# Kernel optimization log

Measured on AMD Instinct MI355X. Metric: run time of the kernel, lower is better.

## Reference

```python
import jax, jax.numpy as jnp
import numpy as np
from jax import lax

NPOINT = 1024
NSAMPLE = 32
RADIUS = 0.2
ALPHA = 0.2  # leaky relu slope


def fps(xyz, npoint):
    """Farthest point sampling. xyz: (B,N,3) -> idx (B,npoint) int32."""
    B, N, _ = xyz.shape
    first = jnp.zeros((B,), dtype=jnp.int32)
    dist0 = jnp.full((B, N), 1e10, dtype=xyz.dtype)

    def step(carry, _):
        dist, last = carry
        lp = jnp.take_along_axis(xyz, last[:, None, None], axis=1)  # (B,1,3)
        nd = jnp.sum((xyz - lp) ** 2, axis=-1)                      # (B,N)
        dist = jnp.minimum(dist, nd)
        nxt = jnp.argmax(dist, axis=-1).astype(jnp.int32)
        return (dist, nxt), nxt

    (_, _), idxs = lax.scan(step, (dist0, first), None, length=npoint - 1)
    return jnp.concatenate([first[:, None], idxs.T], axis=1)  # (B,npoint)


def ball_query(xyz, new_xyz, radius, nsample):
    """First-nsample-in-index-order neighbors within radius. -> idx (B,n,k) int32."""
    B, N, _ = xyz.shape
    d2 = (jnp.sum(new_xyz ** 2, -1)[:, :, None]
          + jnp.sum(xyz ** 2, -1)[:, None, :]
          - 2.0 * jnp.einsum('bnc,bmc->bnm', new_xyz, xyz))  # (B,n,N)
    mask = d2 <= radius * radius
    cand = jnp.where(mask, jnp.arange(N, dtype=jnp.int32)[None, None, :], N)
    srt = jnp.sort(cand, axis=-1)[..., :nsample]             # (B,n,k)
    first = srt[..., :1]
    idx = jnp.where(srt == N, first, srt)                     # pad with first valid
    return jnp.minimum(idx, N - 1).astype(jnp.int32)


def feature_enhance(g, f, gn, fn):
    """g(B,n,3) f(B,n,D) gn(B,n,k,3) fn(B,n,k,D) -> (B,n,k,3*3+1+(D+3)*3+1)."""
    # cal_feature_dis: scale neighbor xyz by exp(-mean |f - fn|)
    d = jnp.abs(f[:, :, None, :] - fn)                        # (B,n,k,D)
    fdist = jnp.exp(-jnp.mean(d, axis=-1, keepdims=True))     # (B,n,k,1)
    gn = gn * fdist                                           # broadcast == torch.repeat
    # avg_g: append softmax-geometry residual to features
    gmean = jnp.mean(gn, axis=2)                              # (B,n,3)
    gd = jnp.abs(jax.nn.softmax(gmean, -1) - jax.nn.softmax(g, -1))  # (B,n,3)
    gd = jnp.broadcast_to(gd[:, :, None, :], fn.shape[:3] + (3,))    # (B,n,k,3)
    fn = jnp.concatenate([fn, gd], axis=-1)                   # (B,n,k,D+3)
    f = jnp.concatenate([f, g], axis=-1)                      # (B,n,D+3)
    pg = jnp.broadcast_to(g[:, :, None, :], gn.shape)
    pf = jnp.broadcast_to(f[:, :, None, :], fn.shape)
    pg1 = pg - gn
    pf1 = pf - fn
    dg = jnp.sqrt(jnp.sum(pg1 ** 2, axis=-1, keepdims=True))
    df = jnp.sqrt(jnp.sum(pf1 ** 2, axis=-1, keepdims=True))
    pg2 = jnp.concatenate([gn, pg, pg1, dg], axis=-1)         # (B,n,k,10)
    pf2 = jnp.concatenate([fn, pf, pf1, df], axis=-1)         # (B,n,k,3(D+3)+1)
    return jnp.concatenate([pg2, pf2], axis=-1)


def hetero_attention(nfn, a, w1, b1):
    """Attention pooling over neighbors. nfn (B,n,k,nc) -> (B,n,c).
    (In the original, dgf->Conv2d 'disf' is computed but never used; omitted.)
    Dropout skipped (eval mode)."""
    e = jax.nn.leaky_relu(jnp.einsum('bnkc,cd->bnkd', nfn, a), ALPHA)
    attn = jax.nn.softmax(e, axis=2)                          # over k (dim=2)
    pooled = jnp.sum(attn * nfn, axis=2)                      # (B,n,nc)
    return jnp.einsum('bnc,oc->bno', pooled, w1) + b1         # 1x1 Conv1d


def setup_inputs() -> dict:
    key = jax.random.key(0)
    k1, k2, k3, k4 = jax.random.split(key, 4)
    B, N, D = 8, 4096, 64
    nc, c_out = 212, 128  # nc = 3*3+1 + 3*(D+3)+1
    xyz = jax.random.uniform(k1, (B, N, 3), dtype=jnp.float32)
    features = jax.random.normal(k2, (B, D, N), dtype=jnp.float32)
    xav = 1.414 * np.sqrt(6.0 / (nc + nc))
    a = jax.random.uniform(k3, (nc, nc), minval=-xav, maxval=xav, dtype=jnp.float32)
    w1 = jax.random.normal(k4, (c_out, nc), dtype=jnp.float32) / np.sqrt(nc)
    b1 = jnp.zeros((c_out,), dtype=jnp.float32)
    return {"xyz": xyz, "features": features, "a": a, "w1": w1, "b1": b1}


def reference(xyz, features, a, w1, b1):
    B, N, _ = xyz.shape
    feat = jnp.transpose(features, (0, 2, 1))                 # (B,N,D)
    fps_idx = fps(xyz, NPOINT)                                # (B,n)
    bidx = jnp.arange(B)[:, None]
    new_xyz = xyz[bidx, fps_idx]                              # (B,n,3)
    f = feat[bidx, fps_idx]                                   # (B,n,D)
    nb_idx = ball_query(xyz, new_xyz, RADIUS, NSAMPLE)        # (B,n,k)
    bidx2 = jnp.arange(B)[:, None, None]
    gn = xyz[bidx2, nb_idx]                                   # (B,n,k,3)
    fn = feat[bidx2, nb_idx]                                  # (B,n,k,D)
    nfn = feature_enhance(new_xyz, f, gn, fn)                 # (B,n,k,212)
    new_features = hetero_attention(nfn, a, w1, b1)           # (B,n,c)
    return new_xyz, jnp.transpose(new_features, (0, 2, 1))    # (B,c,n)
```

## Files before the change

### kernel.cpp

```cpp
#include <hip/hip_runtime.h>
#include <hip/hip_bf16.h>

#define B_    8
#define N_    4096
#define D_    64
#define NP_   1024
#define K_    32
#define NC_   212
#define CO_   128
#define FPS_T 256
#define SVW   72
#define PROWS 139

__device__ __forceinline__ float f32add(float a, float b) { return __fadd_rn(a, b); }
__device__ __forceinline__ float f32sub(float a, float b) { return __fsub_rn(a, b); }
__device__ __forceinline__ float f32mul(float a, float b) { return __fmul_rn(a, b); }

__device__ __forceinline__ void waveArgmaxDpp(float& best, int& bidx) {
#define AMAX_STEP(CTRL)                                                                     \
    {                                                                                       \
        int _v = __builtin_amdgcn_update_dpp(__float_as_int(best), __float_as_int(best),    \
                                             (CTRL), 0xf, 0xf, false);                      \
        int _i = __builtin_amdgcn_update_dpp(bidx, bidx, (CTRL), 0xf, 0xf, false);          \
        float _f = __int_as_float(_v);                                                      \
        if (_f > best || (_f == best && _i < bidx)) { best = _f; bidx = _i; }               \
    }
    AMAX_STEP(0x111);
    AMAX_STEP(0x112);
    AMAX_STEP(0x114);
    AMAX_STEP(0x118);
    AMAX_STEP(0x142);
    AMAX_STEP(0x143);
#undef AMAX_STEP
    best = __int_as_float(__builtin_amdgcn_readlane(__float_as_int(best), 63));
    bidx = __builtin_amdgcn_readlane(bidx, 63);
}

__global__ void fold_kernel(const float* __restrict__ A, float* __restrict__ P) {
    int x = blockIdx.x * 256 + threadIdx.x;
    if (x >= PROWS * NC_) return;
    int r = x / NC_, c = x % NC_;
    float v;
    if      (r < 64)  v = A[(size_t)(77 + r) * NC_ + c] + A[(size_t)(144 + r) * NC_ + c];
    else if (r < 67)  { int j = r - 64;
                        v = (A[(size_t)(3 + j) * NC_ + c] + A[(size_t)(141 + j) * NC_ + c])
                          + A[(size_t)(208 + j) * NC_ + c]; }
    else if (r < 70)  { int j = r - 67;
                        v = A[(size_t)(74 + j) * NC_ + c] - A[(size_t)(208 + j) * NC_ + c]; }
    else if (r < 73)  { int j = r - 70;
                        v = A[(size_t)j * NC_ + c] - A[(size_t)(6 + j) * NC_ + c]; }
    else if (r == 73) v = A[(size_t)9 * NC_ + c];
    else if (r < 138) { int i = r - 74;
                        v = A[(size_t)(10 + i) * NC_ + c] - A[(size_t)(144 + i) * NC_ + c]; }
    else              v = A[(size_t)211 * NC_ + c];
    P[(size_t)r * NC_ + c] = v;
}

__global__ void transpose_kernel(const float* __restrict__ in, float* __restrict__ out) {
    __shared__ float tile[32][33];
    int b  = blockIdx.z;
    int n0 = blockIdx.x * 32, d0 = blockIdx.y * 32;
    const float* src = in  + (size_t)b * D_ * N_;
    float*       dst = out + (size_t)b * N_ * D_;
    int tx = threadIdx.x, ty = threadIdx.y;
#pragma unroll
    for (int r = 0; r < 32; r += 8)
        tile[r + ty][tx] = src[(size_t)(d0 + r + ty) * N_ + n0 + tx];
    __syncthreads();
#pragma unroll
    for (int r = 0; r < 32; r += 8)
        dst[(size_t)(n0 + r + ty) * D_ + d0 + tx] = tile[tx][r + ty];
}

__global__ __launch_bounds__(FPS_T) void fps_kernel(
    const float* __restrict__ xyz,
    int* __restrict__ fpsIdx, float* __restrict__ out0) {
    int b = blockIdx.x;
    const float* P = xyz + (size_t)b * N_ * 3;
    __shared__ float X[N_], Y[N_], Z[N_];
    __shared__ int   hist[NP_];
    __shared__ float redV[2][FPS_T / 64];
    __shared__ int   redI[2][FPS_T / 64];
    int tid = threadIdx.x;
    for (int i = tid; i < N_; i += FPS_T) {
        X[i] = P[i * 3 + 0];
        Y[i] = P[i * 3 + 1];
        Z[i] = P[i * 3 + 2];
    }
    if (tid == 0) hist[0] = 0;
    __syncthreads();

    const int PPT = N_ / FPS_T;
    float px[PPT], py[PPT], pz[PPT], dist[PPT];
#pragma unroll
    for (int c = 0; c < PPT; c++) {
        int j = tid + FPS_T * c;
        px[c] = X[j]; py[c] = Y[j]; pz[c] = Z[j];
        dist[c] = 1e10f;
    }
    int last = 0;
    for (int it = 1; it < NP_; ++it) {
        float lx = X[last], ly = Y[last], lz = Z[last];
        float best = -1.0f; int bidx = 0;
#pragma unroll
        for (int c = 0; c < PPT; c++) {
            float dx = f32sub(px[c], lx), dy = f32sub(py[c], ly), dz = f32sub(pz[c], lz);
            float nd = f32add(f32add(f32mul(dx, dx), f32mul(dy, dy)), f32mul(dz, dz));
            float d  = fminf(dist[c], nd);
            dist[c] = d;
            if (d > best) { best = d; bidx = tid + FPS_T * c; }
        }
        waveArgmaxDpp(best, bidx);
        int par = it & 1;
        if ((tid & 63) == 0) { redV[par][tid >> 6] = best; redI[par][tid >> 6] = bidx; }
        __syncthreads();
        float bv = redV[par][0]; int bi = redI[par][0];
#pragma unroll
        for (int w = 1; w < FPS_T / 64; w++) {
            float ov = redV[par][w]; int oi = redI[par][w];
            if (ov > bv || (ov == bv && oi < bi)) { bv = ov; bi = oi; }
        }
        last = bi;
        if (tid == 0) hist[it] = last;
    }
    __syncthreads();
    for (int i = tid; i < NP_; i += FPS_T) {
        int j = hist[i];
        fpsIdx[b * NP_ + i] = j;
        size_t o = (size_t)(b * NP_ + i) * 3;
        out0[o + 0] = X[j]; out0[o + 1] = Y[j]; out0[o + 2] = Z[j];
    }
}

__global__ __launch_bounds__(256, 4) void fused_kernel(
    const float* __restrict__ featT, const float* __restrict__ xyz,
    const float* __restrict__ newxyz, const int* __restrict__ fpsIdx,
    const float* __restrict__ P, const float* __restrict__ W1,
    const float* __restrict__ B1, float* __restrict__ out1) {
    int q = blockIdx.x;
    int b = q >> 10, n = q & (NP_ - 1);
    int tid = threadIdx.x;
    __shared__ float sV[K_][SVW];
    __shared__ float sF[68];
    __shared__ float sFD[K_];
    __shared__ float sGD[3];
    __shared__ float sGsum[3];
    __shared__ float sPool[NC_];
    __shared__ int   sNb[K_];
    __shared__ int   sCnt;

    if (tid < D_) sF[tid] = featT[((size_t)b * N_ + fpsIdx[q]) * D_ + tid];
    if (tid >= D_ && tid < D_ + 3) sF[tid] = newxyz[q * 3 + (tid - D_)];

    if (tid < 64) {
        int lane = tid;
        if (lane < K_) sNb[lane] = N_ - 1;
        const float* Px = xyz + (size_t)b * N_ * 3;
        float qx = newxyz[q * 3 + 0];
        float qy = newxyz[q * 3 + 1];
        float qz = newxyz[q * 3 + 2];
        float sq = f32add(f32add(f32mul(qx, qx), f32mul(qy, qy)), f32mul(qz, qz));
        const float R2 = (float)(0.2 * 0.2);
        int count = 0;
        for (int base = 0; base < N_ && count < K_; base += 64) {
            int j = base + lane;
            float x = Px[j * 3 + 0];
            float y = Px[j * 3 + 1];
            float z = Px[j * 3 + 2];
            float sxj = f32add(f32add(f32mul(x, x), f32mul(y, y)), f32mul(z, z));
            float dot = __fmaf_rn(qz, z, __fmaf_rn(qy, y, __fmul_rn(qx, x)));
            float d2  = f32sub(f32add(sq, sxj), f32mul(2.0f, dot));
            bool in = (d2 <= R2);
            unsigned long long m = __ballot(in);
            if (in) {
                int pos = count + __popcll(m & ((1ull << lane) - 1ull));
                if (pos < K_) sNb[pos] = j;
            }
            count += __popcll(m);
        }
        if (lane == 0) sCnt = (count < K_) ? count : K_;
    }
    __syncthreads();
    int cnt = sCnt;

    {
        int k = tid >> 3, l = tid & 7;
        int j = (k < cnt || cnt == 0) ? sNb[k] : sNb[0];
        const float* src = featT + ((size_t)b * N_ + j) * D_;
        float4 v0 = *(const float4*)(src + l * 8);
        float4 v1 = *(const float4*)(src + l * 8 + 4);
        float* dst = &sV[k][4 + l * 8];
        dst[0] = v0.x; dst[1] = v0.y; dst[2] = v0.z; dst[3] = v0.w;
        dst[4] = v1.x; dst[5] = v1.y; dst[6] = v1.z; dst[7] = v1.w;
    }
    if (tid < 96) {
        int k = tid / 3, c = tid % 3;
        int j = (k < cnt || cnt == 0) ? sNb[k] : sNb[0];
        sV[k][c] = xyz[((size_t)b * N_ + j) * 3 + c];
        sV[k][69 + c] = 0.f;
    }
    __syncthreads();

    {
        int k = tid >> 3, ds = (tid & 7) * 8;
        float s = 0.f;
#pragma unroll
        for (int j = 0; j < 8; j++) s += fabsf(sF[ds + j] - sV[k][4 + ds + j]);
        s += __shfl_xor(s, 1); s += __shfl_xor(s, 2); s += __shfl_xor(s, 4);
        if ((tid & 7) == 0) sFD[k] = __expf(-s * (1.0f / 64.0f));
    }
    __syncthreads();

    if (tid < 96) {
        int k = tid / 3, c = tid % 3;
        sV[k][c] = sV[k][c] * sFD[k];
    }
    __syncthreads();

    if (tid < K_) {
        int k = tid;
        float a0 = sF[64] - sV[k][0], a1 = sF[65] - sV[k][1], a2 = sF[66] - sV[k][2];
        sV[k][3] = sqrtf(a0 * a0 + a1 * a1 + a2 * a2);
    }
    if (tid >= 64 && tid < 67) {
        int c = tid - 64;
        float s = 0.f;
        for (int k = 0; k < K_; k++) s += sV[k][c];
        sGsum[c] = s;
    }
    __syncthreads();

    if (tid == 0) {
        float m0 = sGsum[0] * (1.f / K_), m1 = sGsum[1] * (1.f / K_), m2 = sGsum[2] * (1.f / K_);
        float mm = fmaxf(m0, fmaxf(m1, m2));
        float e0 = __expf(m0 - mm), e1 = __expf(m1 - mm), e2 = __expf(m2 - mm);
        float inv = 1.f / (e0 + e1 + e2);
        float g0 = sF[64], g1 = sF[65], g2 = sF[66];
        float gm = fmaxf(g0, fmaxf(g1, g2));
        float f0 = __expf(g0 - gm), f1 = __expf(g1 - gm), f2 = __expf(g2 - gm);
        float inv2 = 1.f / (f0 + f1 + f2);
        sGD[0] = fabsf(e0 * inv - f0 * inv2);
        sGD[1] = fabsf(e1 * inv - f1 * inv2);
        sGD[2] = fabsf(e2 * inv - f2 * inv2);
    }
    __syncthreads();

    {
        int k = tid >> 3, l = tid & 7;
        float s = 0.f;
        for (int c = l; c < 67; c += 8) {
            float v = (c < D_) ? (sF[c] - sV[k][4 + c]) : (sF[c] - sGD[c - D_]);
            s += v * v;
        }
        s += __shfl_xor(s, 1); s += __shfl_xor(s, 2); s += __shfl_xor(s, 4);
        if (l == 0) sV[k][68] = sqrtf(s);
    }
    __syncthreads();

    if (tid < NC_) {
        const float* Pc = P + tid;
        float base = 0.f;
#pragma unroll 4
        for (int i = 0; i < 64; i++) base += Pc[(size_t)i * NC_] * sF[i];
#pragma unroll
        for (int j = 0; j < 3; j++) {
            base += Pc[(size_t)(64 + j) * NC_] * sF[64 + j]
                  + Pc[(size_t)(67 + j) * NC_] * sGD[j];
        }

        float acc[K_];
#pragma unroll
        for (int k = 0; k < K_; k++) acc[k] = 0.f;

        {
            float q0 = Pc[(size_t)70 * NC_];
            float q1 = Pc[(size_t)71 * NC_];
            float q2 = Pc[(size_t)72 * NC_];
            float q3 = Pc[(size_t)73 * NC_];
#pragma unroll
            for (int k = 0; k < K_; k++) {
                float4 v = *(const float4*)&sV[k][0];
                acc[k] = fmaf(v.x, q0, fmaf(v.y, q1, fmaf(v.z, q2, fmaf(v.w, q3, acc[k]))));
            }
        }
        for (int gi = 0; gi < 16; gi++) {
            int i0 = gi * 4;
            float q0 = Pc[(size_t)(74 + i0 + 0) * NC_];
            float q1 = Pc[(size_t)(74 + i0 + 1) * NC_];
            float q2 = Pc[(size_t)(74 + i0 + 2) * NC_];
            float q3 = Pc[(size_t)(74 + i0 + 3) * NC_];
#pragma unroll
            for (int k = 0; k < K_; k++) {
                float4 v = *(const float4*)&sV[k][4 + i0];
                acc[k] = fmaf(v.x, q0, fmaf(v.y, q1, fmaf(v.z, q2, fmaf(v.w, q3, acc[k]))));
            }
        }
        {
            float q0 = Pc[(size_t)138 * NC_];
#pragma unroll
            for (int k = 0; k < K_; k++) acc[k] = fmaf(sV[k][68], q0, acc[k]);
        }

        float m = -1e30f;
#pragma unroll
        for (int k = 0; k < K_; k++) {
            float v = base + acc[k];
            v = (v > 0.f) ? v : 0.2f * v;
            acc[k] = v;
            m = fmaxf(m, v);
        }
        float ssum = 0.f;
#pragma unroll
        for (int k = 0; k < K_; k++) { float e = __expf(acc[k] - m); acc[k] = e; ssum += e; }
        float inv = 1.f / ssum;

        int col; float addv; float sgn;
        if      (tid < 3)   { col = tid;       addv = 0.f;           sgn = 1.f; }
        else if (tid < 6)   { col = 0;         addv = sF[61 + tid];  sgn = 0.f; }
        else if (tid < 9)   { col = tid - 6;   addv = sF[58 + tid];  sgn = -1.f; }
        else if (tid == 9)  { col = 3;         addv = 0.f;           sgn = 1.f; }
        else if (tid < 74)  { col = tid - 6;   addv = 0.f;           sgn = 1.f; }
        else if (tid < 77)  { col = 0;         addv = sGD[tid - 74]; sgn = 0.f; }
        else if (tid < 144) { col = 0;         addv = sF[tid - 77];  sgn = 0.f; }
        else if (tid < 208) { col = tid - 140; addv = sF[tid - 144]; sgn = -1.f; }
        else if (tid < 211) { col = 0;         addv = sF[tid - 144] - sGD[tid - 208]; sgn = 0.f; }
        else                { col = 68;        addv = 0.f;           sgn = 1.f; }
        float s = 0.f;
#pragma unroll
        for (int k = 0; k < K_; k++) s += acc[k] * sV[k][col];
        sPool[tid] = addv + sgn * (s * inv);
    }
    __syncthreads();

    if (tid < CO_) {
        const float* w = W1 + (size_t)tid * NC_;
        float accO = 0.f;
        for (int c = 0; c < NC_; c += 4) {
            float4 wv = *(const float4*)(w + c);
            accO += wv.x * sPool[c] + wv.y * sPool[c + 1] + wv.z * sPool[c + 2] + wv.w * sPool[c + 3];
        }
        accO += B1[tid];
        out1[((size_t)b * CO_ + tid) * NP_ + n] = accO;
    }
}

extern "C" void kernel_launch(void* const* d_in, const int* in_sizes, int n_in,
                              void* d_out, int out_size, void* d_ws, size_t ws_size,
                              hipStream_t stream) {
    (void)in_sizes; (void)n_in; (void)out_size; (void)ws_size;
    const float* xyz      = (const float*)d_in[0];
    const float* features = (const float*)d_in[1];
    const float* A        = (const float*)d_in[2];
    const float* W1       = (const float*)d_in[3];
    const float* B1       = (const float*)d_in[4];
    float* out0 = (float*)d_out;
    float* out1 = out0 + (size_t)B_ * NP_ * 3;

    char*  wsB    = (char*)d_ws;
    int*   fpsIdx = (int*)wsB;
    float* P      = (float*)(wsB + 32768);
    float* featT  = (float*)(wsB + 32768 + 118016);

    fold_kernel<<<dim3((PROWS * NC_ + 255) / 256), dim3(256), 0, stream>>>(A, P);
    transpose_kernel<<<dim3(N_ / 32, D_ / 32, B_), dim3(32, 8), 0, stream>>>(features, featT);
    fps_kernel<<<dim3(B_), dim3(FPS_T), 0, stream>>>(xyz, fpsIdx, out0);
    fused_kernel<<<dim3(B_ * NP_), dim3(256), 0, stream>>>(featT, xyz, out0, fpsIdx,
                                                           P, W1, B1, out1);
}
```

Before: 1.218 ms.

## Merge FPS, feature transpose and weight fold into one heterogeneous kernel

Combines the fold, transpose and farthest-point-sampling kernels into a single launch. The first B blocks run FPS and the remaining blocks do the transpose and fold, sharing a union shared-memory buffer. Because FPS uses only 8 blocks, the independent preprocessing work can overlap with it on idle compute units, and two kernel launches are removed. The cost is that every block reserves the large FPS shared-memory footprint, which limits occupancy for the small transpose and fold blocks.

```diff
diff --git a/kernel.cpp b/kernel.cpp
--- a/kernel.cpp
+++ b/kernel.cpp
@@ -11,6 +11,8 @@
 #define FPS_T 256
 #define SVW   72
 #define PROWS 139
+#define NTRB  2048
+#define NFLB  116
 
 __device__ __forceinline__ float f32add(float a, float b) { return __fadd_rn(a, b); }
 __device__ __forceinline__ float f32sub(float a, float b) { return __fsub_rn(a, b); }
@@ -36,58 +38,70 @@
     bidx = __builtin_amdgcn_readlane(bidx, 63);
 }
 
-__global__ void fold_kernel(const float* __restrict__ A, float* __restrict__ P) {
-    int x = blockIdx.x * 256 + threadIdx.x;
-    if (x >= PROWS * NC_) return;
-    int r = x / NC_, c = x % NC_;
-    float v;
-    if      (r < 64)  v = A[(size_t)(77 + r) * NC_ + c] + A[(size_t)(144 + r) * NC_ + c];
-    else if (r < 67)  { int j = r - 64;
-                        v = (A[(size_t)(3 + j) * NC_ + c] + A[(size_t)(141 + j) * NC_ + c])
-                          + A[(size_t)(208 + j) * NC_ + c]; }
-    else if (r < 70)  { int j = r - 67;
-                        v = A[(size_t)(74 + j) * NC_ + c] - A[(size_t)(208 + j) * NC_ + c]; }
-    else if (r < 73)  { int j = r - 70;
-                        v = A[(size_t)j * NC_ + c] - A[(size_t)(6 + j) * NC_ + c]; }
-    else if (r == 73) v = A[(size_t)9 * NC_ + c];
-    else if (r < 138) { int i = r - 74;
-                        v = A[(size_t)(10 + i) * NC_ + c] - A[(size_t)(144 + i) * NC_ + c]; }
-    else              v = A[(size_t)211 * NC_ + c];
-    P[(size_t)r * NC_ + c] = v;
-}
-
-__global__ void transpose_kernel(const float* __restrict__ in, float* __restrict__ out) {
-    __shared__ float tile[32][33];
-    int b  = blockIdx.z;
-    int n0 = blockIdx.x * 32, d0 = blockIdx.y * 32;
-    const float* src = in  + (size_t)b * D_ * N_;
-    float*       dst = out + (size_t)b * N_ * D_;
-    int tx = threadIdx.x, ty = threadIdx.y;
-#pragma unroll
-    for (int r = 0; r < 32; r += 8)
-        tile[r + ty][tx] = src[(size_t)(d0 + r + ty) * N_ + n0 + tx];
-    __syncthreads();
-#pragma unroll
-    for (int r = 0; r < 32; r += 8)
-        dst[(size_t)(n0 + r + ty) * D_ + d0 + tx] = tile[tx][r + ty];
-}
-
-__global__ __launch_bounds__(FPS_T) void fps_kernel(
-    const float* __restrict__ xyz,
-    int* __restrict__ fpsIdx, float* __restrict__ out0) {
+struct FpsSm {
+    float X[N_], Y[N_], Z[N_];
+    int   hist[NP_];
+    float redV[2][FPS_T / 64];
+    int   redI[2][FPS_T / 64];
+};
+struct TrSm { float tile[32][33]; };
+union ComboSm { FpsSm f; TrSm t; };
+
+__global__ __launch_bounds__(FPS_T) void combo_kernel(
+    const float* __restrict__ xyz, const float* __restrict__ features,
+    const float* __restrict__ A,
+    int* __restrict__ fpsIdx, float* __restrict__ out0,
+    float* __restrict__ featT, float* __restrict__ Pm) {
+    __shared__ ComboSm sm;
+    int tid = threadIdx.x;
+
+    if (blockIdx.x >= B_) {
+        int t = blockIdx.x - B_;
+        if (t < NTRB) {
+            int n0 = (t & 127) * 32;
+            int d0 = ((t >> 7) & 1) * 32;
+            int b  = t >> 8;
+            const float* src = features + (size_t)b * D_ * N_;
+            float*       dst = featT    + (size_t)b * N_ * D_;
+            int tx = tid & 31, ty = tid >> 5;
+#pragma unroll
+            for (int r = 0; r < 32; r += 8)
+                sm.t.tile[r + ty][tx] = src[(size_t)(d0 + r + ty) * N_ + n0 + tx];
+            __syncthreads();
+#pragma unroll
+            for (int r = 0; r < 32; r += 8)
+                dst[(size_t)(n0 + r + ty) * D_ + d0 + tx] = sm.t.tile[tx][r + ty];
+        } else {
+            int x = (t - NTRB) * 256 + tid;
+            if (x < PROWS * NC_) {
+                int r = x / NC_, c = x % NC_;
+                float v;
+                if      (r < 64)  v = A[(size_t)(77 + r) * NC_ + c] + A[(size_t)(144 + r) * NC_ + c];
+                else if (r < 67)  { int j = r - 64;
+                                    v = (A[(size_t)(3 + j) * NC_ + c] + A[(size_t)(141 + j) * NC_ + c])
+                                      + A[(size_t)(208 + j) * NC_ + c]; }
+                else if (r < 70)  { int j = r - 67;
+                                    v = A[(size_t)(74 + j) * NC_ + c] - A[(size_t)(208 + j) * NC_ + c]; }
+                else if (r < 73)  { int j = r - 70;
+                                    v = A[(size_t)j * NC_ + c] - A[(size_t)(6 + j) * NC_ + c]; }
+                else if (r == 73) v = A[(size_t)9 * NC_ + c];
+                else if (r < 138) { int i = r - 74;
+                                    v = A[(size_t)(10 + i) * NC_ + c] - A[(size_t)(144 + i) * NC_ + c]; }
+                else              v = A[(size_t)211 * NC_ + c];
+                Pm[(size_t)r * NC_ + c] = v;
+            }
+        }
+        return;
+    }
+
     int b = blockIdx.x;
     const float* P = xyz + (size_t)b * N_ * 3;
-    __shared__ float X[N_], Y[N_], Z[N_];
-    __shared__ int   hist[NP_];
-    __shared__ float redV[2][FPS_T / 64];
-    __shared__ int   redI[2][FPS_T / 64];
-    int tid = threadIdx.x;
     for (int i = tid; i < N_; i += FPS_T) {
-        X[i] = P[i * 3 + 0];
-        Y[i] = P[i * 3 + 1];
-        Z[i] = P[i * 3 + 2];
-    }
-    if (tid == 0) hist[0] = 0;
+        sm.f.X[i] = P[i * 3 + 0];
+        sm.f.Y[i] = P[i * 3 + 1];
+        sm.f.Z[i] = P[i * 3 + 2];
+    }
+    if (tid == 0) sm.f.hist[0] = 0;
     __syncthreads();
 
     const int PPT = N_ / FPS_T;
@@ -95,12 +109,12 @@
 #pragma unroll
     for (int c = 0; c < PPT; c++) {
         int j = tid + FPS_T * c;
-        px[c] = X[j]; py[c] = Y[j]; pz[c] = Z[j];
+        px[c] = sm.f.X[j]; py[c] = sm.f.Y[j]; pz[c] = sm.f.Z[j];
         dist[c] = 1e10f;
     }
     int last = 0;
     for (int it = 1; it < NP_; ++it) {
-        float lx = X[last], ly = Y[last], lz = Z[last];
+        float lx = sm.f.X[last], ly = sm.f.Y[last], lz = sm.f.Z[last];
         float best = -1.0f; int bidx = 0;
 #pragma unroll
         for (int c = 0; c < PPT; c++) {
@@ -112,23 +126,23 @@
         }
         waveArgmaxDpp(best, bidx);
         int par = it & 1;
-        if ((tid & 63) == 0) { redV[par][tid >> 6] = best; redI[par][tid >> 6] = bidx; }
+        if ((tid & 63) == 0) { sm.f.redV[par][tid >> 6] = best; sm.f.redI[par][tid >> 6] = bidx; }
         __syncthreads();
-        float bv = redV[par][0]; int bi = redI[par][0];
+        float bv = sm.f.redV[par][0]; int bi = sm.f.redI[par][0];
 #pragma unroll
         for (int w = 1; w < FPS_T / 64; w++) {
-            float ov = redV[par][w]; int oi = redI[par][w];
+            float ov = sm.f.redV[par][w]; int oi = sm.f.redI[par][w];
             if (ov > bv || (ov == bv && oi < bi)) { bv = ov; bi = oi; }
         }
         last = bi;
-        if (tid == 0) hist[it] = last;
+        if (tid == 0) sm.f.hist[it] = last;
     }
     __syncthreads();
     for (int i = tid; i < NP_; i += FPS_T) {
-        int j = hist[i];
+        int j = sm.f.hist[i];
         fpsIdx[b * NP_ + i] = j;
         size_t o = (size_t)(b * NP_ + i) * 3;
-        out0[o + 0] = X[j]; out0[o + 1] = Y[j]; out0[o + 2] = Z[j];
+        out0[o + 0] = sm.f.X[j]; out0[o + 1] = sm.f.Y[j]; out0[o + 2] = sm.f.Z[j];
     }
 }
 
@@ -361,9 +375,8 @@
     float* P      = (float*)(wsB + 32768);
     float* featT  = (float*)(wsB + 32768 + 118016);
 
-    fold_kernel<<<dim3((PROWS * NC_ + 255) / 256), dim3(256), 0, stream>>>(A, P);
-    transpose_kernel<<<dim3(N_ / 32, D_ / 32, B_), dim3(32, 8), 0, stream>>>(features, featT);
-    fps_kernel<<<dim3(B_), dim3(FPS_T), 0, stream>>>(xyz, fpsIdx, out0);
+    combo_kernel<<<dim3(B_ + NTRB + NFLB), dim3(FPS_T), 0, stream>>>(
+        xyz, features, A, fpsIdx, out0, featT, P);
     fused_kernel<<<dim3(B_ * NP_), dim3(256), 0, stream>>>(featT, xyz, out0, fpsIdx,
                                                            P, W1, B1, out1);
 }
```

Measured after the change: 1.210 ms. About the same (-0.6%).
